# Optimization experiments

Hardware: AMD Instinct MI355X
Metric: run time of the kernel (lower is better)

The kernel has to match this reference:

```python
import jax, jax.numpy as jnp
import numpy as np

NEG = -9e15  # matches torch's -9000000000000000.0 mask value
LN_EPS = 1e-5


def gat_layer(x, adj, W, a, gamma, beta):
    # x: [M, N, Fin], adj: [M, N, N]
    h = x @ W                                  # [M, N, H]
    H = W.shape[1]
    # a([h_i, h_j]) decomposes: e_ij = leakyrelu(h_i.a1 + h_j.a2)
    s_i = h @ a[:H]                            # [M, N]
    s_j = h @ a[H:]                            # [M, N]
    e = jax.nn.leaky_relu(s_i[:, :, None] + s_j[:, None, :], 0.2)
    e = jnp.where(adj > 0, e, NEG)
    att = jax.nn.softmax(e, axis=2)
    hp = jnp.einsum('mij,mjh->mih', att, h)    # bmm aggregation
    mu = hp.mean(-1, keepdims=True)
    var = hp.var(-1, keepdims=True)
    hn = (hp - mu) * jax.lax.rsqrt(var + LN_EPS) * gamma + beta
    return jax.nn.elu(hn)


def lstm_dir(x_seq, Wih, Whh, bih, bhh):
    # x_seq: [B, T, D]; Wih: [D, 4H]; Whh: [H, 4H]; gate order i,f,g,o (torch)
    B = x_seq.shape[0]
    H = Whh.shape[0]
    xg = jnp.einsum('btd,dk->btk', x_seq, Wih) + bih + bhh  # precompute input gates

    def step(carry, xg_t):
        h, c = carry
        g = xg_t + h @ Whh
        i, f, gg, o = jnp.split(g, 4, axis=-1)
        c = jax.nn.sigmoid(f) * c + jax.nn.sigmoid(i) * jnp.tanh(gg)
        h = jax.nn.sigmoid(o) * jnp.tanh(c)
        return (h, c), h

    init = (jnp.zeros((B, H), x_seq.dtype), jnp.zeros((B, H), x_seq.dtype))
    (h_last, _), hs = jax.lax.scan(step, init, jnp.swapaxes(xg, 0, 1))
    return jnp.swapaxes(hs, 0, 1), h_last


def bilstm_layer(x_seq, Wih, Whh, bih, bhh):
    of, hf = lstm_dir(x_seq, Wih[0], Whh[0], bih[0], bhh[0])
    ob, hb = lstm_dir(x_seq[:, ::-1], Wih[1], Whh[1], bih[1], bhh[1])
    return jnp.concatenate([of, ob[:, ::-1]], axis=-1), hf, hb


def setup_inputs() -> dict:
    key = jax.random.key(0)
    ks = jax.random.split(key, 20)
    B, S, N, F, H = 4, 64, 256, 32, 64

    def rn(k, shape, fan_in):
        return jax.random.normal(k, shape, jnp.float32) / np.float32(np.sqrt(fan_in))

    return {
        'x': jax.random.normal(ks[0], (B, S, N, F), jnp.float32),
        'adj': jax.random.randint(ks[1], (B, S, N, N), 0, 2).astype(jnp.float32),
        'gat0_W': rn(ks[2], (F, H), F),
        'gat0_a': rn(ks[3], (2 * H,), 2 * H),
        'gat0_g': jnp.ones((H,), jnp.float32),
        'gat0_b': jnp.zeros((H,), jnp.float32),
        'gat1_W': rn(ks[4], (H, H), H),
        'gat1_a': rn(ks[5], (2 * H,), 2 * H),
        'gat1_g': jnp.ones((H,), jnp.float32),
        'gat1_b': jnp.zeros((H,), jnp.float32),
        'res_W': rn(ks[6], (F, H), F),
        'res_b': jnp.zeros((H,), jnp.float32),
        'alpha_gate': jnp.asarray(0.01, jnp.float32),
        'l0_Wih': rn(ks[7], (2, H, 4 * H), H),
        'l0_Whh': rn(ks[8], (2, H, 4 * H), H),
        'l0_bih': rn(ks[9], (2, 4 * H), H),
        'l0_bhh': rn(ks[10], (2, 4 * H), H),
        'l1_Wih': rn(ks[11], (2, 2 * H, 4 * H), 2 * H),
        'l1_Whh': rn(ks[12], (2, H, 4 * H), H),
        'l1_bih': rn(ks[13], (2, 4 * H), H),
        'l1_bhh': rn(ks[14], (2, 4 * H), H),
        'fc_W': rn(ks[15], (2 * H, 1), 2 * H),
        'fc_b': jnp.zeros((1,), jnp.float32),
    }


def reference(x, adj, gat0_W, gat0_a, gat0_g, gat0_b, gat1_W, gat1_a, gat1_g, gat1_b,
              res_W, res_b, alpha_gate, l0_Wih, l0_Whh, l0_bih, l0_bhh,
              l1_Wih, l1_Whh, l1_bih, l1_bhh, fc_W, fc_b):
    B, S, N, F = x.shape
    x_flat = x.reshape(B * S, N, F)
    adj_flat = adj.reshape(B * S, N, N)

    g = gat_layer(x_flat, adj_flat, gat0_W, gat0_a, gat0_g, gat0_b)
    g = gat_layer(g, adj_flat, gat1_W, gat1_a, gat1_g, gat1_b)

    res = x_flat @ res_W + res_b
    gate = jnp.clip(alpha_gate, 0.0, 1.0)
    comb = res + gate * g                       # [B*S, N, H]
    Hd = comb.shape[-1]

    # [B,S,N,H] -> [B,N,S,H] -> [B*N, S, H]
    seq = comb.reshape(B, S, N, Hd).transpose(0, 2, 1, 3).reshape(B * N, S, Hd)

    o1, _, _ = bilstm_layer(seq, l0_Wih, l0_Whh, l0_bih, l0_bhh)
    _, hf, hb = bilstm_layer(o1, l1_Wih, l1_Whh, l1_bih, l1_bhh)

    final = jnp.concatenate([hf, hb], axis=-1)  # h_n[-2], h_n[-1]
    pred = final @ fc_W + fc_b
    return pred.reshape(B, N, 1)
```

## Files before the change

kernel.cpp:

```cpp
#include <hip/hip_runtime.h>
#include <math.h>

#define BB 4
#define SS 64
#define NN 256
#define FF 32
#define HH 64
#define MM (BB*SS)
#define NSEQ (BB*NN)
#define TT SS
#define MROWS (NSEQ*TT)

__device__ __forceinline__ float fast_rcp(float x) { return __builtin_amdgcn_rcpf(x); }
__device__ __forceinline__ float sigmoid_f(float x) { return fast_rcp(1.0f + __expf(-x)); }
__device__ __forceinline__ float tanh_f(float x) {
    float t = __expf(-2.0f * fabsf(x));
    float r = (1.0f - t) * fast_rcp(1.0f + t);
    return copysignf(r, x);
}

__device__ __forceinline__ void lds_barrier() {
    asm volatile("s_waitcnt lgkmcnt(0)" ::: "memory");
    __builtin_amdgcn_s_barrier();
    __builtin_amdgcn_sched_barrier(0);
}

typedef __bf16 bf16x8 __attribute__((ext_vector_type(8)));
typedef float  f32x4  __attribute__((ext_vector_type(4)));

__device__ __forceinline__ __bf16 bfh(float x) {
    unsigned u = __float_as_uint(x);
    unsigned r = (u + 0x7FFFu + ((u >> 16) & 1u)) >> 16;
    return __builtin_bit_cast(__bf16, (unsigned short)r);
}
__device__ __forceinline__ float bf2f(__bf16 b) {
    unsigned u = ((unsigned)__builtin_bit_cast(unsigned short, b)) << 16;
    return __uint_as_float(u);
}

template<int FIN>
__global__ __launch_bounds__(512) void gat_kernel(
    const float* __restrict__ xin,
    const float* __restrict__ adj,
    const float* __restrict__ W,
    const float* __restrict__ a,
    const float* __restrict__ gamma_, const float* __restrict__ beta_,
    float* __restrict__ gout)
{
    __shared__ __align__(16) float u_f32[256 * 68];
    __shared__ __align__(16) __bf16 p_hi[256 * 40];
    __shared__ __align__(16) __bf16 p_lo[256 * 40];
    __shared__ float s1s[256], s2s[256], srow[256];

    __bf16* F_hi = (__bf16*)u_f32;
    __bf16* F_lo = F_hi + 64 * 264;

    const int m    = blockIdx.x;
    const int tid  = threadIdx.x;
    const int lane = tid & 63;
    const int wv   = tid >> 6;
    const int nl   = lane & 15;
    const int lq   = lane >> 4;
    const int row2 = tid >> 1;
    const int half = tid & 1;

    {
        const int c = tid & 63;
        float wreg[FIN];
#pragma unroll
        for (int f = 0; f < FIN; ++f) wreg[f] = W[f * 64 + c];
        const float* xm = xin + (size_t)m * NN * FIN;
        for (int i0 = 0; i0 < 32; ++i0) {
            int i = (i0 << 3) | wv;
            float acc = 0.0f;
#pragma unroll
            for (int f4 = 0; f4 < FIN / 4; ++f4) {
                float4 xv = *(const float4*)&xm[i * FIN + f4 * 4];
                acc += xv.x * wreg[f4*4] + xv.y * wreg[f4*4+1]
                     + xv.z * wreg[f4*4+2] + xv.w * wreg[f4*4+3];
            }
            u_f32[i * 68 + c] = acc;
        }
    }
    __syncthreads();

    float hr[32];
    {
        const float* hp = &u_f32[row2 * 68 + half * 32];
        float acc1 = 0.0f, acc2 = 0.0f;
#pragma unroll
        for (int c4 = 0; c4 < 8; ++c4) {
            float4 hv = *(const float4*)&hp[c4 * 4];
            hr[c4*4+0] = hv.x; hr[c4*4+1] = hv.y; hr[c4*4+2] = hv.z; hr[c4*4+3] = hv.w;
            float4 av1 = *(const float4*)&a[half * 32 + c4 * 4];
            float4 av2 = *(const float4*)&a[64 + half * 32 + c4 * 4];
            acc1 += hv.x * av1.x + hv.y * av1.y + hv.z * av1.z + hv.w * av1.w;
            acc2 += hv.x * av2.x + hv.y * av2.y + hv.z * av2.z + hv.w * av2.w;
        }
        acc1 += __shfl_xor(acc1, 1);
        acc2 += __shfl_xor(acc2, 1);
        if (half == 0) { s1s[row2] = acc1; s2s[row2] = acc2; }
    }
    __syncthreads();
    {
#pragma unroll
        for (int cc = 0; cc < 32; ++cc) {
            int c = half * 32 + cc;
            __bf16 hh = bfh(hr[cc]);
            F_hi[c * 264 + row2] = hh;
            F_lo[c * 264 + row2] = bfh(hr[cc] - bf2f(hh));
        }
    }

    const float* adjr = adj + ((size_t)m * NN + row2) * NN + half * 16;
    const float s1v = s1s[row2];
    float srow_acc = 0.0f;

    f32x4 acc[2][4];
#pragma unroll
    for (int mt = 0; mt < 2; ++mt)
#pragma unroll
        for (int nt = 0; nt < 4; ++nt)
            acc[mt][nt] = (f32x4){0.0f, 0.0f, 0.0f, 0.0f};

    float4 adjreg[4];
#pragma unroll
    for (int q = 0; q < 4; ++q) adjreg[q] = *(const float4*)&adjr[q * 4];

    for (int ch = 0; ch < 8; ++ch) {
        {
            float pv[16];
#pragma unroll
            for (int q = 0; q < 4; ++q) {
                float4 av = adjreg[q];
                float4 sv = *(const float4*)&s2s[ch * 32 + half * 16 + q * 4];
                float e0 = s1v + sv.x, e1 = s1v + sv.y, e2 = s1v + sv.z, e3 = s1v + sv.w;
                e0 = (e0 > 0.0f) ? e0 : 0.2f * e0;
                e1 = (e1 > 0.0f) ? e1 : 0.2f * e1;
                e2 = (e2 > 0.0f) ? e2 : 0.2f * e2;
                e3 = (e3 > 0.0f) ? e3 : 0.2f * e3;
                float p0 = (av.x > 0.0f) ? __expf(e0) : 0.0f;
                float p1 = (av.y > 0.0f) ? __expf(e1) : 0.0f;
                float p2 = (av.z > 0.0f) ? __expf(e2) : 0.0f;
                float p3 = (av.w > 0.0f) ? __expf(e3) : 0.0f;
                srow_acc += (p0 + p1) + (p2 + p3);
                pv[q*4+0] = p0; pv[q*4+1] = p1; pv[q*4+2] = p2; pv[q*4+3] = p3;
            }
#pragma unroll
            for (int b = 0; b < 2; ++b) {
                bf16x8 h8, l8;
#pragma unroll
                for (int j = 0; j < 8; ++j) {
                    __bf16 hh = bfh(pv[b*8+j]);
                    h8[j] = hh;
                    l8[j] = bfh(pv[b*8+j] - bf2f(hh));
                }
                *(bf16x8*)&p_hi[row2 * 40 + half * 16 + b * 8] = h8;
                *(bf16x8*)&p_lo[row2 * 40 + half * 16 + b * 8] = l8;
            }
        }
        if (ch < 7) {
#pragma unroll
            for (int q = 0; q < 4; ++q)
                adjreg[q] = *(const float4*)&adjr[(ch + 1) * 32 + q * 4];
        }
        lds_barrier();

        bf16x8 pah[2], pal[2], fbh[4], fbl[4];
#pragma unroll
        for (int mt = 0; mt < 2; ++mt) {
            int row = wv * 32 + mt * 16 + nl;
            pah[mt] = *(const bf16x8*)&p_hi[row * 40 + lq * 8];
            pal[mt] = *(const bf16x8*)&p_lo[row * 40 + lq * 8];
        }
#pragma unroll
        for (int nt = 0; nt < 4; ++nt) {
            int fo = (nt * 16 + nl) * 264 + ch * 32 + lq * 8;
            fbh[nt] = *(const bf16x8*)&F_hi[fo];
            fbl[nt] = *(const bf16x8*)&F_lo[fo];
        }
#pragma unroll
        for (int mt = 0; mt < 2; ++mt)
#pragma unroll
            for (int nt = 0; nt < 4; ++nt)
                acc[mt][nt] = __builtin_amdgcn_mfma_f32_16x16x32_bf16(
                    pah[mt], fbh[nt], acc[mt][nt], 0, 0, 0);
#pragma unroll
        for (int mt = 0; mt < 2; ++mt)
#pragma unroll
            for (int nt = 0; nt < 4; ++nt)
                acc[mt][nt] = __builtin_amdgcn_mfma_f32_16x16x32_bf16(
                    pal[mt], fbh[nt], acc[mt][nt], 0, 0, 0);
#pragma unroll
        for (int mt = 0; mt < 2; ++mt)
#pragma unroll
            for (int nt = 0; nt < 4; ++nt)
                acc[mt][nt] = __builtin_amdgcn_mfma_f32_16x16x32_bf16(
                    pah[mt], fbl[nt], acc[mt][nt], 0, 0, 0);

        lds_barrier();
    }

    {
        float sr = srow_acc + __shfl_xor(srow_acc, 1);
        if (half == 0) srow[row2] = sr;
    }
    __syncthreads();

    float gm[4], bt[4];
#pragma unroll
    for (int nt = 0; nt < 4; ++nt) {
        gm[nt] = gamma_[nt * 16 + nl];
        bt[nt] = beta_[nt * 16 + nl];
    }
#pragma unroll
    for (int mt = 0; mt < 2; ++mt) {
#pragma unroll
        for (int r = 0; r < 4; ++r) {
            int row = wv * 32 + mt * 16 + lq * 4 + r;
            float rinv = fast_rcp(srow[row]);
            float v[4];
            float sm = 0.0f, sq = 0.0f;
#pragma unroll
            for (int nt = 0; nt < 4; ++nt) {
                v[nt] = acc[mt][nt][r] * rinv;
                sm += v[nt]; sq += v[nt] * v[nt];
            }
#pragma unroll
            for (int off = 1; off < 16; off <<= 1) {
                sm += __shfl_xor(sm, off);
                sq += __shfl_xor(sq, off);
            }
            float mu  = sm * (1.0f / 64.0f);
            float var = sq * (1.0f / 64.0f) - mu * mu;
            float rs  = rsqrtf(var + 1e-5f);
            float* gp = &gout[((size_t)m * NN + row) * 64];
#pragma unroll
            for (int nt = 0; nt < 4; ++nt) {
                float hn = (v[nt] - mu) * rs * gm[nt] + bt[nt];
                gp[nt * 16 + nl] = (hn > 0.0f) ? hn : (__expf(hn) - 1.0f);
            }
        }
    }
}

__global__ __launch_bounds__(256) void combine_kernel(
    const float* __restrict__ x,
    const float* __restrict__ g1,
    const float* __restrict__ res_W,
    const float* __restrict__ res_b,
    const float* __restrict__ alpha_p,
    float* __restrict__ seqout)
{
    int row = blockIdx.x * 4 + (threadIdx.x >> 6);
    int h = threadIdx.x & 63;
    int mg = row >> 8, n = row & 255;
    int b = mg >> 6, s = mg & 63;
    const float* xr = x + (size_t)row * 32;
    float acc = res_b[h];
#pragma unroll
    for (int f4 = 0; f4 < 8; ++f4) {
        float4 xv = *(const float4*)&xr[f4 * 4];
        acc += xv.x * res_W[(f4*4    ) * 64 + h] + xv.y * res_W[(f4*4 + 1) * 64 + h]
             + xv.z * res_W[(f4*4 + 2) * 64 + h] + xv.w * res_W[(f4*4 + 3) * 64 + h];
    }
    float alpha = fminf(fmaxf(alpha_p[0], 0.0f), 1.0f);
    acc += alpha * g1[(size_t)row * 64 + h];
    seqout[(((size_t)(b * NN + n)) * TT + s) * 64 + h] = acc;
}

template<int K>
__global__ __launch_bounds__(256) void wcvt_kernel(
    const float* __restrict__ Wih, __bf16* __restrict__ Wh, __bf16* __restrict__ Wl)
{
    constexpr int NKC = K / 32;
    int idx = blockIdx.x * 256 + threadIdx.x;
    int j   = idx & 7;
    int nl  = (idx >> 3) & 15;
    int g   = (idx >> 7) & 3;
    int ng  = (idx >> 9) & 15;
    int rest = idx >> 13;
    int kc  = rest & (NKC - 1);
    int dir = rest / NKC;
    int k = kc * 32 + g * 8 + j;
    int n = ng * 16 + nl;
    float x = Wih[((size_t)dir * K + k) * 256 + n];
    __bf16 h = bfh(x);
    Wh[idx] = h;
    Wl[idx] = bfh(x - bf2f(h));
}

__global__ __launch_bounds__(256) void whhcvt_kernel(
    const float* __restrict__ W0, const float* __restrict__ W1,
    __bf16* __restrict__ outw)
{
    int idx = blockIdx.x * 256 + threadIdx.x;
    int lay = idx >> 15;
    int r   = idx & 32767;
    int j   = r & 7;
    int nl  = (r >> 3) & 15;
    int g   = (r >> 7) & 3;
    int ng  = (r >> 9) & 15;
    int rest = r >> 13;
    int kc  = rest & 1;
    int dir = rest >> 1;
    int k = kc * 32 + g * 8 + j;
    int n = ng * 16 + nl;
    const float* W = lay ? W1 : W0;
    float x = W[((size_t)dir * 64 + k) * 256 + n];
    __bf16 h = bfh(x);
    outw[lay * 65536 + r]         = h;
    outw[lay * 65536 + 32768 + r] = bfh(x - bf2f(h));
}

template<int K>
__global__ __launch_bounds__(256, 2) void xg_mfma_kernel(
    const float* __restrict__ A,
    const __bf16* __restrict__ Wh,
    const __bf16* __restrict__ Wl,
    const float* __restrict__ bih,
    const float* __restrict__ bhh,
    float* __restrict__ xg)
{
    constexpr int NKC = K / 32;
    __shared__ __bf16 a_h[2][128 * 32];
    __shared__ __bf16 a_l[2][128 * 32];

    const int tid  = threadIdx.x;
    const int lane = tid & 63;
    const int w    = tid >> 6;
    const int wr   = w >> 1, wc = w & 1;

    int bid = blockIdx.x;
    int wg  = (bid >> 3) | ((bid & 7) << 8);
    int cd  = wg & 3;
    int m0  = (wg >> 2) * 128;
    int dir = cd >> 1;
    const int kq = (cd & 1) * 2 + wc;

    f32x4 acc[4][4];
#pragma unroll
    for (int mi = 0; mi < 4; ++mi)
#pragma unroll
        for (int ni = 0; ni < 4; ++ni)
            acc[mi][ni] = (f32x4){0.0f, 0.0f, 0.0f, 0.0f};

    const int srow = tid >> 1;
    const int g0   = (tid & 1) * 2;
    const float* abase = A + (size_t)(m0 + srow) * K + (tid & 1) * 16;
    const int soff0 = srow * 32 + (( g0      ^ (srow & 3)) * 8);
    const int soff1 = srow * 32 + (((g0 + 1) ^ (srow & 3)) * 8);

    int aoff[4];
#pragma unroll
    for (int mi = 0; mi < 4; ++mi)
        aoff[mi] = (wr * 64 + mi * 16 + (lane & 15)) * 32
                 + (((lane >> 4) ^ (lane & 3)) * 8);

    auto cvtstore = [&](const float* f, int buf) {
        bf16x8 h0, h1, l0, l1;
#pragma unroll
        for (int i = 0; i < 8; ++i) {
            __bf16 ha = bfh(f[i]);
            __bf16 hb = bfh(f[8 + i]);
            h0[i] = ha; l0[i] = bfh(f[i]     - bf2f(ha));
            h1[i] = hb; l1[i] = bfh(f[8 + i] - bf2f(hb));
        }
        *(bf16x8*)&a_h[buf][soff0] = h0;
        *(bf16x8*)&a_h[buf][soff1] = h1;
        *(bf16x8*)&a_l[buf][soff0] = l0;
        *(bf16x8*)&a_l[buf][soff1] = l1;
    };

    {
        float f[16];
#pragma unroll
        for (int i = 0; i < 4; ++i) {
            float4 v = *(const float4*)(abase + i * 4);
            f[i*4+0] = v.x; f[i*4+1] = v.y; f[i*4+2] = v.z; f[i*4+3] = v.w;
        }
        cvtstore(f, 0);
    }
    lds_barrier();

    int buf = 0;
    for (int kc = 0; kc < NKC; ++kc) {
        float f[16];
        if (kc + 1 < NKC) {
#pragma unroll
            for (int i = 0; i < 4; ++i) {
                float4 v = *(const float4*)(abase + (kc + 1) * 32 + i * 4);
                f[i*4+0] = v.x; f[i*4+1] = v.y; f[i*4+2] = v.z; f[i*4+3] = v.w;
            }
        }
        bf16x8 bh[4], bl[4];
#pragma unroll
        for (int ni = 0; ni < 4; ++ni) {
            size_t fb = ((size_t)((dir * NKC + kc) * 16 + ni * 4 + kq)) * 512 + lane * 8;
            bh[ni] = *(const bf16x8*)(Wh + fb);
            bl[ni] = *(const bf16x8*)(Wl + fb);
        }
        bf16x8 ah[4], al[4];
#pragma unroll
        for (int mi = 0; mi < 4; ++mi) {
            ah[mi] = *(const bf16x8*)&a_h[buf][aoff[mi]];
            al[mi] = *(const bf16x8*)&a_l[buf][aoff[mi]];
        }
#pragma unroll
        for (int mi = 0; mi < 4; ++mi)
#pragma unroll
            for (int ni = 0; ni < 4; ++ni)
                acc[mi][ni] = __builtin_amdgcn_mfma_f32_16x16x32_bf16(
                    ah[mi], bh[ni], acc[mi][ni], 0, 0, 0);
#pragma unroll
        for (int mi = 0; mi < 4; ++mi)
#pragma unroll
            for (int ni = 0; ni < 4; ++ni)
                acc[mi][ni] = __builtin_amdgcn_mfma_f32_16x16x32_bf16(
                    al[mi], bh[ni], acc[mi][ni], 0, 0, 0);
#pragma unroll
        for (int mi = 0; mi < 4; ++mi)
#pragma unroll
            for (int ni = 0; ni < 4; ++ni)
                acc[mi][ni] = __builtin_amdgcn_mfma_f32_16x16x32_bf16(
                    ah[mi], bl[ni], acc[mi][ni], 0, 0, 0);

        if (kc + 1 < NKC) cvtstore(f, buf ^ 1);
        lds_barrier();
        buf ^= 1;
    }

    const int kcol = kq * 16 + (lane & 15);
    float bias4[4];
#pragma unroll
    for (int g = 0; g < 4; ++g)
        bias4[g] = bih[dir * 256 + g * 64 + kcol] + bhh[dir * 256 + g * 64 + kcol];
#pragma unroll
    for (int mi = 0; mi < 4; ++mi) {
        int mrow = m0 + wr * 64 + mi * 16 + ((lane >> 4) << 2);
#pragma unroll
        for (int r = 0; r < 4; ++r) {
            float4 v = make_float4(acc[mi][0][r] + bias4[0], acc[mi][1][r] + bias4[1],
                                   acc[mi][2][r] + bias4[2], acc[mi][3][r] + bias4[3]);
            *(float4*)&xg[((size_t)dir * MROWS + mrow + r) * 256 + kcol * 4] = v;
        }
    }
}

__global__ __launch_bounds__(256, 2) void lstm_rec_kernel(
    const float* __restrict__ xg,
    const __bf16* __restrict__ whhf,
    float* __restrict__ out,
    int write_all)
{
    const int tid  = threadIdx.x;
    const int wv   = tid >> 6;
    const int lane = tid & 63;
    const int nl   = lane & 15;
    const int lq   = lane >> 4;

    const int bid  = blockIdx.x;
    const int dir  = bid & 1;
    const int seq0 = (bid >> 1) * 4;

    const __bf16* wh = whhf;
    const __bf16* wl = whhf + 32768;
    bf16x8 bh[2][4], bl[2][4];
#pragma unroll
    for (int kc = 0; kc < 2; ++kc)
#pragma unroll
        for (int g = 0; g < 4; ++g) {
            size_t fb = ((size_t)((dir * 2 + kc) * 16 + g * 4 + wv)) * 512 + lane * 8;
            bh[kc][g] = *(const bf16x8*)(wh + fb);
            bl[kc][g] = *(const bf16x8*)(wl + fb);
        }

    __shared__ __align__(16) __bf16 h_hi[2048];
    __shared__ __align__(16) __bf16 h_lo[2048];
    {
        uint4 z = {0, 0, 0, 0};
        *(uint4*)&h_hi[tid * 8] = z;
        *(uint4*)&h_lo[tid * 8] = z;
    }

    const int k   = wv * 16 + nl;
    const int g8k = k >> 3;

    float c = 0.0f;
    float4 xa = {}, xb = {};

    const float* pxg = xg + (((size_t)dir * NSEQ + seq0 + lq) * TT
                             + (dir ? (TT - 1) : 0)) * 256 + k * 4;
    const int dstep = dir ? -256 : 256;
    float* pout = out + (((size_t)(seq0 + lq)) * TT + (dir ? (TT - 1) : 0)) * 128
                + dir * 64 + k;
    const int ostep = dir ? -128 : 128;

    auto load_xg = [&](float4& d) {
        d = *(const float4*)pxg;
        pxg += dstep;
    };

    int buf = 0;
    auto step_body = [&](int step, float4& xcur, float4& xnext, bool pre) {
        const int aof0 = buf * 1024 + nl * 64 + (((0 + lq) ^ (nl & 7)) * 8);
        const int aof1 = buf * 1024 + nl * 64 + (((4 + lq) ^ (nl & 7)) * 8);
        bf16x8 ah0 = *(const bf16x8*)&h_hi[aof0];
        bf16x8 ah1 = *(const bf16x8*)&h_hi[aof1];
        bf16x8 al0 = *(const bf16x8*)&h_lo[aof0];
        bf16x8 al1 = *(const bf16x8*)&h_lo[aof1];

        if (pre) load_xg(xnext);

        f32x4 acc[4];
#pragma unroll
        for (int g = 0; g < 4; ++g) acc[g] = (f32x4){0.0f, 0.0f, 0.0f, 0.0f};
#pragma unroll
        for (int g = 0; g < 4; ++g)
            acc[g] = __builtin_amdgcn_mfma_f32_16x16x32_bf16(ah0, bh[0][g], acc[g], 0, 0, 0);
#pragma unroll
        for (int g = 0; g < 4; ++g)
            acc[g] = __builtin_amdgcn_mfma_f32_16x16x32_bf16(ah1, bh[1][g], acc[g], 0, 0, 0);
#pragma unroll
        for (int g = 0; g < 4; ++g)
            acc[g] = __builtin_amdgcn_mfma_f32_16x16x32_bf16(al0, bh[0][g], acc[g], 0, 0, 0);
#pragma unroll
        for (int g = 0; g < 4; ++g)
            acc[g] = __builtin_amdgcn_mfma_f32_16x16x32_bf16(al1, bh[1][g], acc[g], 0, 0, 0);
#pragma unroll
        for (int g = 0; g < 4; ++g)
            acc[g] = __builtin_amdgcn_mfma_f32_16x16x32_bf16(ah0, bl[0][g], acc[g], 0, 0, 0);
#pragma unroll
        for (int g = 0; g < 4; ++g)
            acc[g] = __builtin_amdgcn_mfma_f32_16x16x32_bf16(ah1, bl[1][g], acc[g], 0, 0, 0);

        float pre4[4];
#pragma unroll
        for (int g = 0; g < 4; ++g) {
            float b0 = __shfl(acc[g][0], nl);
            float b1 = __shfl(acc[g][1], nl);
            float b2 = __shfl(acc[g][2], nl);
            float b3 = __shfl(acc[g][3], nl);
            float v01 = (lq & 1) ? b1 : b0;
            float v23 = (lq & 1) ? b3 : b2;
            pre4[g] = (lq & 2) ? v23 : v01;
        }

        float iv = sigmoid_f(pre4[0] + xcur.x);
        float fv = sigmoid_f(pre4[1] + xcur.y);
        float gv = tanh_f  (pre4[2] + xcur.z);
        float ov = sigmoid_f(pre4[3] + xcur.w);
        c = fv * c + iv * gv;
        float h = ov * tanh_f(c);
        int off = (buf ^ 1) * 1024 + lq * 64 + ((g8k ^ lq) * 8) + (k & 7);
        __bf16 hh = bfh(h);
        h_hi[off] = hh;
        h_lo[off] = bfh(h - bf2f(hh));
        if (write_all)
            pout[0] = h;
        else if (step == TT - 1)
            out[(size_t)(seq0 + lq) * 128 + dir * 64 + k] = h;
        pout += ostep;
        lds_barrier();
        buf ^= 1;
    };

    load_xg(xa);
    lds_barrier();

    for (int step = 0; step < TT; step += 2) {
        step_body(step,     xa, xb, true);
        step_body(step + 1, xb, xa, step + 2 < TT);
    }
}

__global__ __launch_bounds__(256) void fc_kernel(
    const float* __restrict__ fin,
    const float* __restrict__ fc_W,
    const float* __restrict__ fc_b,
    float* __restrict__ outp)
{
    int s = blockIdx.x * 256 + threadIdx.x;
    const float* fr = fin + (size_t)s * 128;
    float acc = fc_b[0];
#pragma unroll
    for (int k4 = 0; k4 < 32; ++k4) {
        float4 fv = *(const float4*)&fr[k4 * 4];
        float4 wv2 = *(const float4*)&fc_W[k4 * 4];
        acc += fv.x * wv2.x + fv.y * wv2.y + fv.z * wv2.z + fv.w * wv2.w;
    }
    outp[s] = acc;
}

extern "C" void kernel_launch(void* const* d_in, const int* in_sizes, int n_in,
                              void* d_out, int out_size, void* d_ws, size_t ws_size,
                              hipStream_t stream) {
    const float* x       = (const float*)d_in[0];
    const float* adj     = (const float*)d_in[1];
    const float* gat0_W  = (const float*)d_in[2];
    const float* gat0_a  = (const float*)d_in[3];
    const float* gat0_g  = (const float*)d_in[4];
    const float* gat0_b  = (const float*)d_in[5];
    const float* gat1_W  = (const float*)d_in[6];
    const float* gat1_a  = (const float*)d_in[7];
    const float* gat1_g  = (const float*)d_in[8];
    const float* gat1_b  = (const float*)d_in[9];
    const float* res_W   = (const float*)d_in[10];
    const float* res_b   = (const float*)d_in[11];
    const float* alpha_g = (const float*)d_in[12];
    const float* l0_Wih  = (const float*)d_in[13];
    const float* l0_Whh  = (const float*)d_in[14];
    const float* l0_bih  = (const float*)d_in[15];
    const float* l0_bhh  = (const float*)d_in[16];
    const float* l1_Wih  = (const float*)d_in[17];
    const float* l1_Whh  = (const float*)d_in[18];
    const float* l1_bih  = (const float*)d_in[19];
    const float* l1_bhh  = (const float*)d_in[20];
    const float* fc_W    = (const float*)d_in[21];
    const float* fc_b    = (const float*)d_in[22];

    float* ws = (float*)d_ws;
    float* g0    = ws;
    float* g1    = ws + 4194304;
    float* seq   = ws + 8388608;
    float* xg    = ws + 12582912;
    float* fin   = ws + 46137344;
    float* o1    = ws;

    __bf16* w0h = (__bf16*)(ws + 46137344);
    __bf16* w0l = w0h + 2 * 64 * 256;
    __bf16* w1h = w0l + 2 * 64 * 256;
    __bf16* w1l = w1h + 2 * 128 * 256;

    __bf16* whhf = (__bf16*)seq;

    wcvt_kernel<64><<<128, 256, 0, stream>>>(l0_Wih, w0h, w0l);
    wcvt_kernel<128><<<256, 256, 0, stream>>>(l1_Wih, w1h, w1l);
    gat_kernel<32><<<MM, 512, 0, stream>>>(x, adj, gat0_W, gat0_a, gat0_g, gat0_b, g0);
    gat_kernel<64><<<MM, 512, 0, stream>>>(g0, adj, gat1_W, gat1_a, gat1_g, gat1_b, g1);
    combine_kernel<<<(BB*SS*NN)/4, 256, 0, stream>>>(x, g1, res_W, res_b, alpha_g, seq);
    xg_mfma_kernel<64><<<2048, 256, 0, stream>>>(seq, w0h, w0l, l0_bih, l0_bhh, xg);
    whhcvt_kernel<<<256, 256, 0, stream>>>(l0_Whh, l1_Whh, whhf);
    lstm_rec_kernel<<<512, 256, 0, stream>>>(xg, whhf, o1, 1);
    xg_mfma_kernel<128><<<2048, 256, 0, stream>>>(o1, w1h, w1l, l1_bih, l1_bhh, xg);
    lstm_rec_kernel<<<512, 256, 0, stream>>>(xg, whhf + 65536, fin, 0);
    fc_kernel<<<NSEQ/256, 256, 0, stream>>>(fin, fc_W, fc_b, (float*)d_out);
}
```

Measured before the change: 442.7 us.

## Fuse LSTM input-gate projection into recurrent kernel, dropping the xg buffer

```diff
diff --git a/kernel.cpp b/kernel.cpp
--- a/kernel.cpp
+++ b/kernel.cpp
@@ -9,7 +9,6 @@
 #define MM (BB*SS)
 #define NSEQ (BB*NN)
 #define TT SS
-#define MROWS (NSEQ*TT)
 
 __device__ __forceinline__ float fast_rcp(float x) { return __builtin_amdgcn_rcpf(x); }
 __device__ __forceinline__ float sigmoid_f(float x) { return fast_rcp(1.0f + __expf(-x)); }
@@ -314,145 +313,19 @@
 }
 
 template<int K>
-__global__ __launch_bounds__(256, 2) void xg_mfma_kernel(
-    const float* __restrict__ A,
-    const __bf16* __restrict__ Wh,
-    const __bf16* __restrict__ Wl,
+__global__ __launch_bounds__(256, 2) void lstm_fused_kernel(
+    const float* __restrict__ xin,
+    const __bf16* __restrict__ whhf,
+    const __bf16* __restrict__ wih_h,
+    const __bf16* __restrict__ wih_l,
     const float* __restrict__ bih,
     const float* __restrict__ bhh,
-    float* __restrict__ xg)
-{
-    constexpr int NKC = K / 32;
-    __shared__ __bf16 a_h[2][128 * 32];
-    __shared__ __bf16 a_l[2][128 * 32];
-
-    const int tid  = threadIdx.x;
-    const int lane = tid & 63;
-    const int w    = tid >> 6;
-    const int wr   = w >> 1, wc = w & 1;
-
-    int bid = blockIdx.x;
-    int wg  = (bid >> 3) | ((bid & 7) << 8);
-    int cd  = wg & 3;
-    int m0  = (wg >> 2) * 128;
-    int dir = cd >> 1;
-    const int kq = (cd & 1) * 2 + wc;
-
-    f32x4 acc[4][4];
-#pragma unroll
-    for (int mi = 0; mi < 4; ++mi)
-#pragma unroll
-        for (int ni = 0; ni < 4; ++ni)
-            acc[mi][ni] = (f32x4){0.0f, 0.0f, 0.0f, 0.0f};
-
-    const int srow = tid >> 1;
-    const int g0   = (tid & 1) * 2;
-    const float* abase = A + (size_t)(m0 + srow) * K + (tid & 1) * 16;
-    const int soff0 = srow * 32 + (( g0      ^ (srow & 3)) * 8);
-    const int soff1 = srow * 32 + (((g0 + 1) ^ (srow & 3)) * 8);
-
-    int aoff[4];
-#pragma unroll
-    for (int mi = 0; mi < 4; ++mi)
-        aoff[mi] = (wr * 64 + mi * 16 + (lane & 15)) * 32
-                 + (((lane >> 4) ^ (lane & 3)) * 8);
-
-    auto cvtstore = [&](const float* f, int buf) {
-        bf16x8 h0, h1, l0, l1;
-#pragma unroll
-        for (int i = 0; i < 8; ++i) {
-            __bf16 ha = bfh(f[i]);
-            __bf16 hb = bfh(f[8 + i]);
-            h0[i] = ha; l0[i] = bfh(f[i]     - bf2f(ha));
-            h1[i] = hb; l1[i] = bfh(f[8 + i] - bf2f(hb));
-        }
-        *(bf16x8*)&a_h[buf][soff0] = h0;
-        *(bf16x8*)&a_h[buf][soff1] = h1;
-        *(bf16x8*)&a_l[buf][soff0] = l0;
-        *(bf16x8*)&a_l[buf][soff1] = l1;
-    };
-
-    {
-        float f[16];
-#pragma unroll
-        for (int i = 0; i < 4; ++i) {
-            float4 v = *(const float4*)(abase + i * 4);
-            f[i*4+0] = v.x; f[i*4+1] = v.y; f[i*4+2] = v.z; f[i*4+3] = v.w;
-        }
-        cvtstore(f, 0);
-    }
-    lds_barrier();
-
-    int buf = 0;
-    for (int kc = 0; kc < NKC; ++kc) {
-        float f[16];
-        if (kc + 1 < NKC) {
-#pragma unroll
-            for (int i = 0; i < 4; ++i) {
-                float4 v = *(const float4*)(abase + (kc + 1) * 32 + i * 4);
-                f[i*4+0] = v.x; f[i*4+1] = v.y; f[i*4+2] = v.z; f[i*4+3] = v.w;
-            }
-        }
-        bf16x8 bh[4], bl[4];
-#pragma unroll
-        for (int ni = 0; ni < 4; ++ni) {
-            size_t fb = ((size_t)((dir * NKC + kc) * 16 + ni * 4 + kq)) * 512 + lane * 8;
-            bh[ni] = *(const bf16x8*)(Wh + fb);
-            bl[ni] = *(const bf16x8*)(Wl + fb);
-        }
-        bf16x8 ah[4], al[4];
-#pragma unroll
-        for (int mi = 0; mi < 4; ++mi) {
-            ah[mi] = *(const bf16x8*)&a_h[buf][aoff[mi]];
-            al[mi] = *(const bf16x8*)&a_l[buf][aoff[mi]];
-        }
-#pragma unroll
-        for (int mi = 0; mi < 4; ++mi)
-#pragma unroll
-            for (int ni = 0; ni < 4; ++ni)
-                acc[mi][ni] = __builtin_amdgcn_mfma_f32_16x16x32_bf16(
-                    ah[mi], bh[ni], acc[mi][ni], 0, 0, 0);
-#pragma unroll
-        for (int mi = 0; mi < 4; ++mi)
-#pragma unroll
-            for (int ni = 0; ni < 4; ++ni)
-                acc[mi][ni] = __builtin_amdgcn_mfma_f32_16x16x32_bf16(
-                    al[mi], bh[ni], acc[mi][ni], 0, 0, 0);
-#pragma unroll
-        for (int mi = 0; mi < 4; ++mi)
-#pragma unroll
-            for (int ni = 0; ni < 4; ++ni)
-                acc[mi][ni] = __builtin_amdgcn_mfma_f32_16x16x32_bf16(
-                    ah[mi], bl[ni], acc[mi][ni], 0, 0, 0);
-
-        if (kc + 1 < NKC) cvtstore(f, buf ^ 1);
-        lds_barrier();
-        buf ^= 1;
-    }
-
-    const int kcol = kq * 16 + (lane & 15);
-    float bias4[4];
-#pragma unroll
-    for (int g = 0; g < 4; ++g)
-        bias4[g] = bih[dir * 256 + g * 64 + kcol] + bhh[dir * 256 + g * 64 + kcol];
-#pragma unroll
-    for (int mi = 0; mi < 4; ++mi) {
-        int mrow = m0 + wr * 64 + mi * 16 + ((lane >> 4) << 2);
-#pragma unroll
-        for (int r = 0; r < 4; ++r) {
-            float4 v = make_float4(acc[mi][0][r] + bias4[0], acc[mi][1][r] + bias4[1],
-                                   acc[mi][2][r] + bias4[2], acc[mi][3][r] + bias4[3]);
-            *(float4*)&xg[((size_t)dir * MROWS + mrow + r) * 256 + kcol * 4] = v;
-        }
-    }
-}
-
-__global__ __launch_bounds__(256, 2) void lstm_rec_kernel(
-    const float* __restrict__ xg,
-    const __bf16* __restrict__ whhf,
     float* __restrict__ out,
     int write_all)
 {
+    constexpr int NKC = K / 32;
+    constexpr int XPT = (4 * K) / 256;
+
     const int tid  = threadIdx.x;
     const int wv   = tid >> 6;
     const int lane = tid & 63;
@@ -465,74 +338,151 @@
 
     const __bf16* wh = whhf;
     const __bf16* wl = whhf + 32768;
-    bf16x8 bh[2][4], bl[2][4];
+    bf16x8 hbh[2][4], hbl[2][4];
 #pragma unroll
     for (int kc = 0; kc < 2; ++kc)
 #pragma unroll
         for (int g = 0; g < 4; ++g) {
             size_t fb = ((size_t)((dir * 2 + kc) * 16 + g * 4 + wv)) * 512 + lane * 8;
-            bh[kc][g] = *(const bf16x8*)(wh + fb);
-            bl[kc][g] = *(const bf16x8*)(wl + fb);
-        }
+            hbh[kc][g] = *(const bf16x8*)(wh + fb);
+            hbl[kc][g] = *(const bf16x8*)(wl + fb);
+        }
+    bf16x8 wbh[NKC][4];
+#pragma unroll
+    for (int kc = 0; kc < NKC; ++kc)
+#pragma unroll
+        for (int g = 0; g < 4; ++g) {
+            size_t fb = ((size_t)((dir * NKC + kc) * 16 + g * 4 + wv)) * 512 + lane * 8;
+            wbh[kc][g] = *(const bf16x8*)(wih_h + fb);
+        }
+    const __bf16* wlb[4];
+#pragma unroll
+    for (int g = 0; g < 4; ++g)
+        wlb[g] = wih_l + ((size_t)(dir * NKC) * 16 + g * 4 + wv) * 512 + lane * 8;
 
     __shared__ __align__(16) __bf16 h_hi[2048];
     __shared__ __align__(16) __bf16 h_lo[2048];
+    __shared__ __align__(16) __bf16 x_hi[32 * K];
+    __shared__ __align__(16) __bf16 x_lo[32 * K];
     {
         uint4 z = {0, 0, 0, 0};
         *(uint4*)&h_hi[tid * 8] = z;
         *(uint4*)&h_lo[tid * 8] = z;
-    }
+#pragma unroll
+        for (int i = 0; i < K / 64; ++i) {
+            *(uint4*)&x_hi[tid * 8 + i * 2048] = z;
+            *(uint4*)&x_lo[tid * 8 + i * 2048] = z;
+        }
+    }
+    __syncthreads();
 
     const int k   = wv * 16 + nl;
     const int g8k = k >> 3;
 
+    float bias4[4];
+#pragma unroll
+    for (int g = 0; g < 4; ++g)
+        bias4[g] = bih[dir * 256 + g * 64 + k] + bhh[dir * 256 + g * 64 + k];
+
     float c = 0.0f;
-    float4 xa = {}, xb = {};
-
-    const float* pxg = xg + (((size_t)dir * NSEQ + seq0 + lq) * TT
-                             + (dir ? (TT - 1) : 0)) * 256 + k * 4;
-    const int dstep = dir ? -256 : 256;
-    float* pout = out + (((size_t)(seq0 + lq)) * TT + (dir ? (TT - 1) : 0)) * 128
-                + dir * 64 + k;
+
+    int xoff[XPT];
+    const float* px[XPT];
+    const int trow0 = dir ? (TT - 1) : 0;
+    const int dstepx = dir ? -K : K;
+#pragma unroll
+    for (int i = 0; i < XPT; ++i) {
+        int v = tid + i * 256;
+        int s = v / K, kx = v & (K - 1);
+        xoff[i] = s * K + (((kx >> 3) ^ s) * 8) + (kx & 7);
+        px[i] = xin + ((size_t)(seq0 + s) * TT + trow0) * K + kx;
+    }
+    auto issue_x = [&](float (&d)[XPT]) {
+#pragma unroll
+        for (int i = 0; i < XPT; ++i) { d[i] = *px[i]; px[i] += dstepx; }
+    };
+    auto write_x = [&](float (&d)[XPT], int pbuf) {
+#pragma unroll
+        for (int i = 0; i < XPT; ++i) {
+            __bf16 hh = bfh(d[i]);
+            x_hi[pbuf * 16 * K + xoff[i]] = hh;
+            x_lo[pbuf * 16 * K + xoff[i]] = bfh(d[i] - bf2f(hh));
+        }
+    };
+
+    float* pout = out + (((size_t)(seq0 + lq)) * TT + trow0) * 128 + dir * 64 + k;
     const int ostep = dir ? -128 : 128;
 
-    auto load_xg = [&](float4& d) {
-        d = *(const float4*)pxg;
-        pxg += dstep;
-    };
+    float xr0[XPT];
+    issue_x(xr0);
+    write_x(xr0, 0);
+    float xrA[XPT], xrB[XPT];
+    issue_x(xrA);
+    lds_barrier();
 
     int buf = 0;
-    auto step_body = [&](int step, float4& xcur, float4& xnext, bool pre) {
-        const int aof0 = buf * 1024 + nl * 64 + (((0 + lq) ^ (nl & 7)) * 8);
-        const int aof1 = buf * 1024 + nl * 64 + (((4 + lq) ^ (nl & 7)) * 8);
-        bf16x8 ah0 = *(const bf16x8*)&h_hi[aof0];
-        bf16x8 ah1 = *(const bf16x8*)&h_hi[aof1];
-        bf16x8 al0 = *(const bf16x8*)&h_lo[aof0];
-        bf16x8 al1 = *(const bf16x8*)&h_lo[aof1];
-
-        if (pre) load_xg(xnext);
+    auto step_body = [&](int step, float (&xcur)[XPT], float (&xnext)[XPT]) {
+        const int aofh0 = buf * 1024 + nl * 64 + (((0 + lq) ^ (nl & 7)) * 8);
+        const int aofh1 = buf * 1024 + nl * 64 + (((4 + lq) ^ (nl & 7)) * 8);
+        bf16x8 ah0 = *(const bf16x8*)&h_hi[aofh0];
+        bf16x8 ah1 = *(const bf16x8*)&h_hi[aofh1];
+        bf16x8 al0 = *(const bf16x8*)&h_lo[aofh0];
+        bf16x8 al1 = *(const bf16x8*)&h_lo[aofh1];
+        bf16x8 xh[NKC], xl[NKC];
+#pragma unroll
+        for (int kc = 0; kc < NKC; ++kc) {
+            int xo = buf * 16 * K + nl * K + ((((kc * 4) + lq) ^ (nl & 7)) * 8);
+            xh[kc] = *(const bf16x8*)&x_hi[xo];
+            xl[kc] = *(const bf16x8*)&x_lo[xo];
+        }
+
+        bf16x8 wblq[2][4];
+#pragma unroll
+        for (int g = 0; g < 4; ++g)
+            wblq[0][g] = *(const bf16x8*)(wlb[g]);
+        if (step + 2 < TT) issue_x(xnext);
 
         f32x4 acc[4];
 #pragma unroll
         for (int g = 0; g < 4; ++g) acc[g] = (f32x4){0.0f, 0.0f, 0.0f, 0.0f};
 #pragma unroll
         for (int g = 0; g < 4; ++g)
-            acc[g] = __builtin_amdgcn_mfma_f32_16x16x32_bf16(ah0, bh[0][g], acc[g], 0, 0, 0);
-#pragma unroll
-        for (int g = 0; g < 4; ++g)
-            acc[g] = __builtin_amdgcn_mfma_f32_16x16x32_bf16(ah1, bh[1][g], acc[g], 0, 0, 0);
-#pragma unroll
-        for (int g = 0; g < 4; ++g)
-            acc[g] = __builtin_amdgcn_mfma_f32_16x16x32_bf16(al0, bh[0][g], acc[g], 0, 0, 0);
-#pragma unroll
-        for (int g = 0; g < 4; ++g)
-            acc[g] = __builtin_amdgcn_mfma_f32_16x16x32_bf16(al1, bh[1][g], acc[g], 0, 0, 0);
-#pragma unroll
-        for (int g = 0; g < 4; ++g)
-            acc[g] = __builtin_amdgcn_mfma_f32_16x16x32_bf16(ah0, bl[0][g], acc[g], 0, 0, 0);
-#pragma unroll
-        for (int g = 0; g < 4; ++g)
-            acc[g] = __builtin_amdgcn_mfma_f32_16x16x32_bf16(ah1, bl[1][g], acc[g], 0, 0, 0);
+            acc[g] = __builtin_amdgcn_mfma_f32_16x16x32_bf16(ah0, hbh[0][g], acc[g], 0, 0, 0);
+#pragma unroll
+        for (int g = 0; g < 4; ++g)
+            acc[g] = __builtin_amdgcn_mfma_f32_16x16x32_bf16(ah1, hbh[1][g], acc[g], 0, 0, 0);
+#pragma unroll
+        for (int g = 0; g < 4; ++g)
+            acc[g] = __builtin_amdgcn_mfma_f32_16x16x32_bf16(al0, hbh[0][g], acc[g], 0, 0, 0);
+#pragma unroll
+        for (int g = 0; g < 4; ++g)
+            acc[g] = __builtin_amdgcn_mfma_f32_16x16x32_bf16(al1, hbh[1][g], acc[g], 0, 0, 0);
+#pragma unroll
+        for (int g = 0; g < 4; ++g)
+            acc[g] = __builtin_amdgcn_mfma_f32_16x16x32_bf16(ah0, hbl[0][g], acc[g], 0, 0, 0);
+#pragma unroll
+        for (int g = 0; g < 4; ++g)
+            acc[g] = __builtin_amdgcn_mfma_f32_16x16x32_bf16(ah1, hbl[1][g], acc[g], 0, 0, 0);
+#pragma unroll
+        for (int kc = 0; kc < NKC; ++kc)
+#pragma unroll
+            for (int g = 0; g < 4; ++g)
+                acc[g] = __builtin_amdgcn_mfma_f32_16x16x32_bf16(xh[kc], wbh[kc][g], acc[g], 0, 0, 0);
+#pragma unroll
+        for (int kc = 0; kc < NKC; ++kc)
+#pragma unroll
+            for (int g = 0; g < 4; ++g)
+                acc[g] = __builtin_amdgcn_mfma_f32_16x16x32_bf16(xl[kc], wbh[kc][g], acc[g], 0, 0, 0);
+#pragma unroll
+        for (int kc = 0; kc < NKC; ++kc) {
+            if (kc + 1 < NKC)
+#pragma unroll
+                for (int g = 0; g < 4; ++g)
+                    wblq[(kc + 1) & 1][g] = *(const bf16x8*)(wlb[g] + (kc + 1) * 8192);
+#pragma unroll
+            for (int g = 0; g < 4; ++g)
+                acc[g] = __builtin_amdgcn_mfma_f32_16x16x32_bf16(xh[kc], wblq[kc & 1][g], acc[g], 0, 0, 0);
+        }
 
         float pre4[4];
 #pragma unroll
@@ -546,10 +496,10 @@
             pre4[g] = (lq & 2) ? v23 : v01;
         }
 
-        float iv = sigmoid_f(pre4[0] + xcur.x);
-        float fv = sigmoid_f(pre4[1] + xcur.y);
-        float gv = tanh_f  (pre4[2] + xcur.z);
-        float ov = sigmoid_f(pre4[3] + xcur.w);
+        float iv = sigmoid_f(pre4[0] + bias4[0]);
+        float fv = sigmoid_f(pre4[1] + bias4[1]);
+        float gv = tanh_f  (pre4[2] + bias4[2]);
+        float ov = sigmoid_f(pre4[3] + bias4[3]);
         c = fv * c + iv * gv;
         float h = ov * tanh_f(c);
         int off = (buf ^ 1) * 1024 + lq * 64 + ((g8k ^ lq) * 8) + (k & 7);
@@ -561,16 +511,14 @@
         else if (step == TT - 1)
             out[(size_t)(seq0 + lq) * 128 + dir * 64 + k] = h;
         pout += ostep;
+        if (step + 1 < TT) write_x(xcur, buf ^ 1);
         lds_barrier();
         buf ^= 1;
     };
 
-    load_xg(xa);
-    lds_barrier();
-
     for (int step = 0; step < TT; step += 2) {
-        step_body(step,     xa, xb, true);
-        step_body(step + 1, xb, xa, step + 2 < TT);
+        step_body(step,     xrA, xrB);
+        step_body(step + 1, xrB, xrA);
     }
 }
 
@@ -623,26 +571,24 @@
     float* g0    = ws;
     float* g1    = ws + 4194304;
     float* seq   = ws + 8388608;
-    float* xg    = ws + 12582912;
+    float* o1    = ws;
     float* fin   = ws + 46137344;
-    float* o1    = ws;
-
-    __bf16* w0h = (__bf16*)(ws + 46137344);
-    __bf16* w0l = w0h + 2 * 64 * 256;
-    __bf16* w1h = w0l + 2 * 64 * 256;
-    __bf16* w1l = w1h + 2 * 128 * 256;
-
-    __bf16* whhf = (__bf16*)seq;
+
+    __bf16* w0h  = (__bf16*)(ws + 12582912);
+    __bf16* w0l  = w0h + 32768;
+    __bf16* w1h  = w0l + 32768;
+    __bf16* w1l  = w1h + 65536;
+    __bf16* whhf = w1l + 65536;
 
     wcvt_kernel<64><<<128, 256, 0, stream>>>(l0_Wih, w0h, w0l);
     wcvt_kernel<128><<<256, 256, 0, stream>>>(l1_Wih, w1h, w1l);
+    whhcvt_kernel<<<256, 256, 0, stream>>>(l0_Whh, l1_Whh, whhf);
     gat_kernel<32><<<MM, 512, 0, stream>>>(x, adj, gat0_W, gat0_a, gat0_g, gat0_b, g0);
     gat_kernel<64><<<MM, 512, 0, stream>>>(g0, adj, gat1_W, gat1_a, gat1_g, gat1_b, g1);
     combine_kernel<<<(BB*SS*NN)/4, 256, 0, stream>>>(x, g1, res_W, res_b, alpha_g, seq);
-    xg_mfma_kernel<64><<<2048, 256, 0, stream>>>(seq, w0h, w0l, l0_bih, l0_bhh, xg);
-    whhcvt_kernel<<<256, 256, 0, stream>>>(l0_Whh, l1_Whh, whhf);
-    lstm_rec_kernel<<<512, 256, 0, stream>>>(xg, whhf, o1, 1);
-    xg_mfma_kernel<128><<<2048, 256, 0, stream>>>(o1, w1h, w1l, l1_bih, l1_bhh, xg);
-    lstm_rec_kernel<<<512, 256, 0, stream>>>(xg, whhf + 65536, fin, 0);
+    lstm_fused_kernel<64><<<512, 256, 0, stream>>>(seq, whhf, w0h, w0l,
+                                                   l0_bih, l0_bhh, o1, 1);
+    lstm_fused_kernel<128><<<512, 256, 0, stream>>>(o1, whhf + 65536, w1h, w1l,
+                                                    l1_bih, l1_bhh, fin, 0);
     fc_kernel<<<NSEQ/256, 256, 0, stream>>>(fin, fc_W, fc_b, (float*)d_out);
 }
```

New measurement: 594.6 us. 34.3% more time.
